# Kernel optimization log

Hardware: AMD Instinct MI355X
Metric: run time of the kernel (lower is better)

Reference implementation:

```python
import jax, jax.numpy as jnp
import numpy as np

B, T, V, E_DIM, M_DIM, H = 32, 256, 10000, 300, 128, 256


def setup_inputs() -> dict:
    key = jax.random.key(0)
    ks = jax.random.split(key, 8)
    sc = 0.05
    words = jax.random.randint(ks[0], (B, T), 0, V)            # int token ids, 0 = pad
    midis = jax.random.normal(ks[1], (B, T, M_DIM), dtype=jnp.float32)
    E  = jax.random.normal(ks[2], (V, E_DIM), dtype=jnp.float32) * sc   # embedding table
    Wm = jax.random.normal(ks[3], (M_DIM, E_DIM), dtype=jnp.float32) * sc  # midi Dense
    bm = jnp.zeros((E_DIM,), jnp.float32)
    Wx = jax.random.normal(ks[4], (E_DIM, 3 * H), dtype=jnp.float32) * sc  # GRU input kernel [z|r|h]
    bx = jnp.zeros((3 * H,), jnp.float32)
    U  = jax.random.normal(ks[5], (H, 3 * H), dtype=jnp.float32) * sc      # GRU recurrent kernel
    bu = jnp.zeros((3 * H,), jnp.float32)                                  # recurrent bias (reset_after)
    Wo = jax.random.normal(ks[6], (H, V), dtype=jnp.float32) * sc          # output Dense
    bo = jnp.zeros((V,), jnp.float32)
    return {"words": words, "midis": midis, "E": E, "Wm": Wm, "bm": bm,
            "Wx": Wx, "bx": bx, "U": U, "bu": bu, "Wo": Wo, "bo": bo}


def _gru_masked(x, mask, Wx, bx, U, bu):
    """Keras GRU (reset_after=True) with mask carry-through. x: [B,T,E], mask: [B,T] bool."""
    gx = x @ Wx + bx                      # [B,T,3H] precomputed input gates
    gx_t = jnp.swapaxes(gx, 0, 1)         # [T,B,3H]
    m_t = mask.T                          # [T,B]
    h0 = jnp.zeros((x.shape[0], H), x.dtype)

    def step(h, inp):
        g, m = inp
        gh = h @ U + bu                   # [B,3H]
        xz, xr, xn = jnp.split(g, 3, axis=-1)
        hz, hr, hn = jnp.split(gh, 3, axis=-1)
        z = jax.nn.sigmoid(xz + hz)
        r = jax.nn.sigmoid(xr + hr)
        n = jnp.tanh(xn + r * hn)         # reset_after: r applied to recurrent projection
        h_new = z * h + (1.0 - z) * n
        h_new = jnp.where(m[:, None], h_new, h)  # masked step: carry state/output
        return h_new, h_new

    h_last, seq = jax.lax.scan(step, h0, (gx_t, m_t))
    return jnp.swapaxes(seq, 0, 1), h_last  # [B,T,H], [B,H]


def reference(words, midis, E, Wm, bm, Wx, bx, U, bu, Wo, bo):
    mask = words != 0                      # Embedding(mask_zero=True).compute_mask
    x = E[words] + (midis @ Wm + bm)       # [B,T,E] fused embedding + dense add
    seq, _ = _gru_masked(x, mask, Wx, bx, U, bu)
    return seq @ Wo + bo                   # [B,T,V] logits
```

## Files before the change

### kernel.cpp

```cpp
#include <hip/hip_runtime.h>
#include <hip/hip_fp16.h>

typedef unsigned short ushort_t;
typedef short bf16x8 __attribute__((ext_vector_type(8)));
typedef float f32x4 __attribute__((ext_vector_type(4)));

#define B_SZ 32
#define T_SZ 256
#define V_SZ 10000
#define E_DIM 300
#define M_DIM 128
#define H_SZ 256

__device__ __forceinline__ ushort_t f2bf(float f) {
  unsigned u = __float_as_uint(f);
  unsigned r = u + 0x7fffu + ((u >> 16) & 1u);
  return (ushort_t)(r >> 16);
}

__global__ void k_cast_bf16(const float* __restrict__ in, ushort_t* __restrict__ out, int n) {
  int i = blockIdx.x * blockDim.x + threadIdx.x;
  if (i < n) out[i] = f2bf(in[i]);
}

template <int MODE>
__global__ void k_transpose_cast(const float* __restrict__ in, ushort_t* __restrict__ out,
                                 int R, int C, int Rp, int Cp) {
  __shared__ float tile[32][33];
  int c0 = blockIdx.x * 32, r0 = blockIdx.y * 32;
  int tx = threadIdx.x, ty = threadIdx.y;
#pragma unroll
  for (int i = 0; i < 32; i += 8) {
    int r = r0 + ty + i, c = c0 + tx;
    tile[ty + i][tx] = (r < R && c < C) ? in[(size_t)r * C + c] : 0.f;
  }
  __syncthreads();
#pragma unroll
  for (int i = 0; i < 32; i += 8) {
    int c = c0 + ty + i, r = r0 + tx;
    if (c < Cp && r < Rp) {
      float v = tile[tx][ty + i];
      if (MODE == 0) {
        out[(size_t)c * Rp + r] = f2bf(v);
      } else {
        __half h = __float2half(v);
        out[(size_t)c * Rp + r] = *(ushort_t*)&h;
      }
    }
  }
}

__global__ void k_xfuse(const float* __restrict__ xtmp, const float* __restrict__ E,
                        const int* __restrict__ words, ushort_t* __restrict__ xb) {
  int m = blockIdx.x;
  int kp = threadIdx.x;
  int w = words[m];
  float v = 0.f;
  if (kp < E_DIM) v = xtmp[(size_t)m * 320 + kp] + E[(size_t)w * E_DIM + kp];
  xb[(size_t)m * 320 + kp] = f2bf(v);
}

__global__ __launch_bounds__(256, 2) void k_gemm_bt(
    const ushort_t* __restrict__ A, const ushort_t* __restrict__ BT,
    const float* __restrict__ bias, float* __restrict__ C,
    int M, int K, int Nreal, int ldc) {
  __shared__ __align__(16) char smem[32768];
  char* As = smem;
  char* Bs = smem + 16384;
  const int tid = threadIdx.x;
  const int lane = tid & 63;
  const int w = tid >> 6;
  const int wr = w >> 1, wc = w & 1;
  const int m0 = blockIdx.x * 128;
  const int n0 = blockIdx.y * 128;

  f32x4 acc[4][4];
#pragma unroll
  for (int i = 0; i < 4; ++i)
#pragma unroll
    for (int j = 0; j < 4; ++j) acc[i][j] = (f32x4){0.f, 0.f, 0.f, 0.f};

  const int srow = tid >> 3;
  const int sc16 = tid & 7;

  for (int k0 = 0; k0 < K; k0 += 64) {
    __syncthreads();
#pragma unroll
    for (int it = 0; it < 4; ++it) {
      int row = srow + it * 32;
      int slot = sc16 ^ (row & 7);
      bf16x8 va = *(const bf16x8*)(A + (size_t)(m0 + row) * K + k0 + sc16 * 8);
      *(bf16x8*)(As + row * 128 + (slot << 4)) = va;
      bf16x8 vb = *(const bf16x8*)(BT + (size_t)(n0 + row) * K + k0 + sc16 * 8);
      *(bf16x8*)(Bs + row * 128 + (slot << 4)) = vb;
    }
    __syncthreads();

    bf16x8 af[4][2], bfr[4][2];
#pragma unroll
    for (int mi = 0; mi < 4; ++mi) {
      int r = wr * 64 + mi * 16 + (lane & 15);
#pragma unroll
      for (int kk = 0; kk < 2; ++kk) {
        int c16 = kk * 4 + (lane >> 4);
        af[mi][kk] = *(const bf16x8*)(As + r * 128 + ((c16 ^ (r & 7)) << 4));
      }
    }
#pragma unroll
    for (int ni = 0; ni < 4; ++ni) {
      int r = wc * 64 + ni * 16 + (lane & 15);
#pragma unroll
      for (int kk = 0; kk < 2; ++kk) {
        int c16 = kk * 4 + (lane >> 4);
        bfr[ni][kk] = *(const bf16x8*)(Bs + r * 128 + ((c16 ^ (r & 7)) << 4));
      }
    }
#pragma unroll
    for (int mi = 0; mi < 4; ++mi)
#pragma unroll
      for (int ni = 0; ni < 4; ++ni)
#pragma unroll
        for (int kk = 0; kk < 2; ++kk)
          acc[mi][ni] = __builtin_amdgcn_mfma_f32_16x16x32_bf16(af[mi][kk], bfr[ni][kk],
                                                                acc[mi][ni], 0, 0, 0);
  }

  const int rbase = m0 + wr * 64 + (lane >> 4) * 4;
  const int cbase = n0 + wc * 64 + (lane & 15);
#pragma unroll
  for (int ni = 0; ni < 4; ++ni) {
    int n = cbase + ni * 16;
    if (n < Nreal) {
      float bn = bias[n];
#pragma unroll
      for (int mi = 0; mi < 4; ++mi) {
#pragma unroll
        for (int rg = 0; rg < 4; ++rg) {
          int mrow = rbase + mi * 16 + rg;
          C[(size_t)mrow * ldc + n] = acc[mi][ni][rg] + bn;
        }
      }
    }
  }
}

__global__ __launch_bounds__(768, 3) void k_gru(
    const float* __restrict__ gx, const ushort_t* __restrict__ UT,
    const float* __restrict__ bu, const int* __restrict__ words,
    ushort_t* __restrict__ seqb) {
  const int b = blockIdx.x;
  const int j = threadIdx.x;
  __shared__ __align__(16) __half hbuf[H_SZ];
  __shared__ float rbuf[H_SZ];
  __shared__ float hnbuf[H_SZ];

  const __half2* Uc = (const __half2*)(UT + (size_t)j * H_SZ);
  __half2 Ur[128];
#pragma unroll
  for (int k = 0; k < 128; ++k) Ur[k] = Uc[k];
  const float bu_j = bu[j];

  float h_old = 0.f;
  if (j < H_SZ) hbuf[j] = __float2half(0.f);
  __syncthreads();

  const float4* hb4 = (const float4*)hbuf;
  for (int t = 0; t < T_SZ; ++t) {
    const size_t row = (size_t)b * T_SZ + t;
    const float* gxr = gx + row * 768;
    const int wv = words[row];
    float gxv = gxr[j];
    float xn = (j < H_SZ) ? gxr[2 * H_SZ + j] : 0.f;

    __half2 a0 = __float2half2_rn(0.f), a1 = a0;
#pragma unroll
    for (int k4 = 0; k4 < 32; ++k4) {
      float4 hv = hb4[k4];
      const __half2* hp = (const __half2*)(&hv);
      a0 = __hfma2(Ur[4 * k4 + 0], hp[0], a0);
      a1 = __hfma2(Ur[4 * k4 + 1], hp[1], a1);
      a0 = __hfma2(Ur[4 * k4 + 2], hp[2], a0);
      a1 = __hfma2(Ur[4 * k4 + 3], hp[3], a1);
    }
    float2 s0 = __half22float2(a0), s1 = __half22float2(a1);
    float gh = s0.x + s0.y + s1.x + s1.y + bu_j;

    float z = 0.f;
    if (j >= 2 * H_SZ) {
      hnbuf[j - 2 * H_SZ] = gh;
    } else if (j >= H_SZ) {
      rbuf[j - H_SZ] = 1.f / (1.f + __expf(-(gxv + gh)));
    } else {
      z = 1.f / (1.f + __expf(-(gxv + gh)));
    }
    __syncthreads();
    if (j < H_SZ) {
      float ni = xn + rbuf[j] * hnbuf[j];
      float n = 2.f / (1.f + __expf(-2.f * ni)) - 1.f;
      float hnew = (wv != 0) ? (z * h_old + (1.f - z) * n) : h_old;
      h_old = hnew;
      seqb[row * H_SZ + j] = f2bf(hnew);
      hbuf[j] = __float2half(hnew);
    }
    __syncthreads();
  }
}

extern "C" void kernel_launch(void* const* d_in, const int* in_sizes, int n_in,
                              void* d_out, int out_size, void* d_ws, size_t ws_size,
                              hipStream_t stream) {
  const int*   words = (const int*)d_in[0];
  const float* midis = (const float*)d_in[1];
  const float* E     = (const float*)d_in[2];
  const float* Wm    = (const float*)d_in[3];
  const float* bm    = (const float*)d_in[4];
  const float* Wx    = (const float*)d_in[5];
  const float* bx    = (const float*)d_in[6];
  const float* U     = (const float*)d_in[7];
  const float* bu    = (const float*)d_in[8];
  const float* Wo    = (const float*)d_in[9];
  const float* bo    = (const float*)d_in[10];
  float* out = (float*)d_out;

  const int MT = B_SZ * T_SZ;
  size_t off = 0;
  auto alloc = [&](size_t bytes) -> void* {
    void* p = (char*)d_ws + off;
    off += (bytes + 255) & ~(size_t)255;
    return p;
  };
  ushort_t* mid_b = (ushort_t*)alloc((size_t)MT * 128 * 2);
  ushort_t* WmT   = (ushort_t*)alloc((size_t)384 * 128 * 2);
  float*    xtmp  = (float*)   alloc((size_t)MT * 320 * 4);
  ushort_t* x_b   = (ushort_t*)alloc((size_t)MT * 320 * 2);
  ushort_t* WxT   = (ushort_t*)alloc((size_t)768 * 320 * 2);
  float*    gx    = (float*)   alloc((size_t)MT * 768 * 4);
  ushort_t* UT    = (ushort_t*)alloc((size_t)768 * 256 * 2);
  ushort_t* seq_b = (ushort_t*)alloc((size_t)MT * 256 * 2);
  ushort_t* WoT   = (ushort_t*)alloc((size_t)10112 * 256 * 2);
  (void)ws_size;

  k_cast_bf16<<<(MT * 128 + 255) / 256, 256, 0, stream>>>(midis, mid_b, MT * 128);
  k_transpose_cast<0><<<dim3(12, 4),  dim3(32, 8), 0, stream>>>(Wm, WmT, 128, 300, 128, 384);
  k_transpose_cast<0><<<dim3(24, 10), dim3(32, 8), 0, stream>>>(Wx, WxT, 300, 768, 320, 768);
  k_transpose_cast<0><<<dim3(316, 8), dim3(32, 8), 0, stream>>>(Wo, WoT, 256, 10000, 256, 10112);
  k_transpose_cast<1><<<dim3(24, 8),  dim3(32, 8), 0, stream>>>(U, UT, 256, 768, 256, 768);

  k_gemm_bt<<<dim3(64, 3), 256, 0, stream>>>(mid_b, WmT, bm, xtmp, MT, 128, 300, 320);
  k_xfuse<<<MT, 320, 0, stream>>>(xtmp, E, words, x_b);
  k_gemm_bt<<<dim3(64, 6), 256, 0, stream>>>(x_b, WxT, bx, gx, MT, 320, 768, 768);
  k_gru<<<B_SZ, 768, 0, stream>>>(gx, UT, bu, words, seq_b);
  k_gemm_bt<<<dim3(64, 79), 256, 0, stream>>>(seq_b, WoT, bo, out, MT, 256, 10000, 10000);
}
```

Measured before the change: 506.7 us.

## Prefetch GRU gate inputs, double-buffer hidden state, use fdot2 with fp32 accumulation

In the recurrent GRU kernel, the next timestep's precomputed input gates are loaded one step ahead, so global-memory latency overlaps with the current matvec. Word ids are staged into shared memory once per block. The hidden-state buffer is double-buffered. The packed-half FMAs are replaced by v_dot2 fp32-accumulating dot products across four independent accumulators, which improves accuracy and instruction-level parallelism but adds register pressure from the prefetched values.

New measurement: 502.9 us. About the same (-0.8%).

```diff
diff --git a/kernel.cpp b/kernel.cpp
--- a/kernel.cpp
+++ b/kernel.cpp
@@ -4,6 +4,7 @@
 typedef unsigned short ushort_t;
 typedef short bf16x8 __attribute__((ext_vector_type(8)));
 typedef float f32x4 __attribute__((ext_vector_type(4)));
+typedef _Float16 h2v __attribute__((ext_vector_type(2)));
 
 #define B_SZ 32
 #define T_SZ 256
@@ -150,40 +151,47 @@
     ushort_t* __restrict__ seqb) {
   const int b = blockIdx.x;
   const int j = threadIdx.x;
-  __shared__ __align__(16) __half hbuf[H_SZ];
+  __shared__ __align__(16) _Float16 hbuf[2][H_SZ];
   __shared__ float rbuf[H_SZ];
   __shared__ float hnbuf[H_SZ];
-
-  const __half2* Uc = (const __half2*)(UT + (size_t)j * H_SZ);
-  __half2 Ur[128];
+  __shared__ int words_s[T_SZ];
+
+  const h2v* Uc = (const h2v*)(UT + (size_t)j * H_SZ);
+  h2v Ur[128];
 #pragma unroll
   for (int k = 0; k < 128; ++k) Ur[k] = Uc[k];
   const float bu_j = bu[j];
 
+  if (j < H_SZ) hbuf[0][j] = (_Float16)0.f;
+  if (j < T_SZ) words_s[j] = words[b * T_SZ + j];
+  __syncthreads();
+
+  const float* gxp = gx + (size_t)b * T_SZ * 768;
+  float gxv = gxp[j];
+  float xn = (j < H_SZ) ? gxp[2 * H_SZ + j] : 0.f;
   float h_old = 0.f;
-  if (j < H_SZ) hbuf[j] = __float2half(0.f);
-  __syncthreads();
-
-  const float4* hb4 = (const float4*)hbuf;
+  int p = 0;
+
   for (int t = 0; t < T_SZ; ++t) {
-    const size_t row = (size_t)b * T_SZ + t;
-    const float* gxr = gx + row * 768;
-    const int wv = words[row];
-    float gxv = gxr[j];
-    float xn = (j < H_SZ) ? gxr[2 * H_SZ + j] : 0.f;
-
-    __half2 a0 = __float2half2_rn(0.f), a1 = a0;
+    float gxv_n = 0.f, xn_n = 0.f;
+    if (t + 1 < T_SZ) {
+      const float* gxr1 = gxp + (size_t)(t + 1) * 768;
+      gxv_n = gxr1[j];
+      if (j < H_SZ) xn_n = gxr1[2 * H_SZ + j];
+    }
+
+    const float4* hb4 = (const float4*)hbuf[p];
+    float a0 = 0.f, a1 = 0.f, a2 = 0.f, a3 = 0.f;
 #pragma unroll
     for (int k4 = 0; k4 < 32; ++k4) {
       float4 hv = hb4[k4];
-      const __half2* hp = (const __half2*)(&hv);
-      a0 = __hfma2(Ur[4 * k4 + 0], hp[0], a0);
-      a1 = __hfma2(Ur[4 * k4 + 1], hp[1], a1);
-      a0 = __hfma2(Ur[4 * k4 + 2], hp[2], a0);
-      a1 = __hfma2(Ur[4 * k4 + 3], hp[3], a1);
-    }
-    float2 s0 = __half22float2(a0), s1 = __half22float2(a1);
-    float gh = s0.x + s0.y + s1.x + s1.y + bu_j;
+      const h2v* hp = (const h2v*)(&hv);
+      a0 = __builtin_amdgcn_fdot2(Ur[4 * k4 + 0], hp[0], a0, false);
+      a1 = __builtin_amdgcn_fdot2(Ur[4 * k4 + 1], hp[1], a1, false);
+      a2 = __builtin_amdgcn_fdot2(Ur[4 * k4 + 2], hp[2], a2, false);
+      a3 = __builtin_amdgcn_fdot2(Ur[4 * k4 + 3], hp[3], a3, false);
+    }
+    float gh = (a0 + a1) + (a2 + a3) + bu_j;
 
     float z = 0.f;
     if (j >= 2 * H_SZ) {
@@ -197,12 +205,15 @@
     if (j < H_SZ) {
       float ni = xn + rbuf[j] * hnbuf[j];
       float n = 2.f / (1.f + __expf(-2.f * ni)) - 1.f;
-      float hnew = (wv != 0) ? (z * h_old + (1.f - z) * n) : h_old;
+      float hnew = (words_s[t] != 0) ? (z * h_old + (1.f - z) * n) : h_old;
       h_old = hnew;
-      seqb[row * H_SZ + j] = f2bf(hnew);
-      hbuf[j] = __float2half(hnew);
-    }
-    __syncthreads();
+      seqb[((size_t)b * T_SZ + t) * H_SZ + j] = f2bf(hnew);
+      hbuf[p ^ 1][j] = (_Float16)hnew;
+    }
+    __syncthreads();
+    gxv = gxv_n;
+    xn = xn_n;
+    p ^= 1;
   }
 }
 
```

## Compute GRU recurrent matvec with fp16 MFMA and register-resident U fragments

Applied to the files above, without the earlier changes.

The per-step h@U product in the GRU kernel moves from per-thread half2 FMA dot products over 768 threads to MFMA 16x16x32 f16 instructions across 8 waves. The hidden state sits as row 0 of a padded 16-row LDS tile, and U fragments stay in registers. Gate math is merged into the first 256 threads, words are staged in LDS, and next-step gx values are prefetched to hide global latency. The MFMA wastes 15 of 16 rows, and its fp32 accumulation changes numerics slightly compared with the old fp16 accumulation.

New measurement: 464.6 us. 8.3% less time.

```diff
diff --git a/kernel.cpp b/kernel.cpp
--- a/kernel.cpp
+++ b/kernel.cpp
@@ -4,6 +4,7 @@
 typedef unsigned short ushort_t;
 typedef short bf16x8 __attribute__((ext_vector_type(8)));
 typedef float f32x4 __attribute__((ext_vector_type(4)));
+typedef _Float16 f16x8 __attribute__((ext_vector_type(8)));
 
 #define B_SZ 32
 #define T_SZ 256
@@ -144,65 +145,98 @@
   }
 }
 
-__global__ __launch_bounds__(768, 3) void k_gru(
+__global__ __launch_bounds__(512, 2) void k_gru(
     const float* __restrict__ gx, const ushort_t* __restrict__ UT,
     const float* __restrict__ bu, const int* __restrict__ words,
     ushort_t* __restrict__ seqb) {
   const int b = blockIdx.x;
-  const int j = threadIdx.x;
-  __shared__ __align__(16) __half hbuf[H_SZ];
-  __shared__ float rbuf[H_SZ];
-  __shared__ float hnbuf[H_SZ];
-
-  const __half2* Uc = (const __half2*)(UT + (size_t)j * H_SZ);
-  __half2 Ur[128];
-#pragma unroll
-  for (int k = 0; k < 128; ++k) Ur[k] = Uc[k];
-  const float bu_j = bu[j];
-
+  const int tid = threadIdx.x;
+  const int lane = tid & 63;
+  const int w = tid >> 6;
+
+  __shared__ __align__(16) _Float16 hlds[16 * 256];
+  __shared__ float ghbuf[768];
+  __shared__ int words_s[T_SZ];
+
+  for (int i = tid; i < 16 * 256; i += 512) hlds[i] = (_Float16)0.f;
+  if (tid < T_SZ) words_s[tid] = words[b * T_SZ + tid];
+
+  f16x8 Ufrag[6][8];
+  {
+    const int n0 = w * 96;
+    const ushort_t* src = UT + (size_t)(n0 + (lane & 15)) * 256 + (lane >> 4) * 8;
+#pragma unroll
+    for (int ni = 0; ni < 6; ++ni) {
+#pragma unroll
+      for (int kk = 0; kk < 8; ++kk)
+        Ufrag[ni][kk] = *(const f16x8*)(src + (size_t)ni * 16 * 256 + kk * 32);
+    }
+  }
+  float buz = 0.f, bur = 0.f, bun = 0.f;
+  if (tid < H_SZ) {
+    buz = bu[tid];
+    bur = bu[H_SZ + tid];
+    bun = bu[2 * H_SZ + tid];
+  }
+  __syncthreads();
+
+  const float* gxp = gx + (size_t)b * T_SZ * 768;
+  float gxz = 0.f, gxr = 0.f, gxn = 0.f;
+  if (tid < H_SZ) {
+    gxz = gxp[tid];
+    gxr = gxp[H_SZ + tid];
+    gxn = gxp[2 * H_SZ + tid];
+  }
   float h_old = 0.f;
-  if (j < H_SZ) hbuf[j] = __float2half(0.f);
-  __syncthreads();
-
-  const float4* hb4 = (const float4*)hbuf;
+
+  const int arow = lane & 15;
+  const int abase = arow * 512;
+  const int asub = lane >> 4;
+  const int aswz = arow & 7;
+
   for (int t = 0; t < T_SZ; ++t) {
-    const size_t row = (size_t)b * T_SZ + t;
-    const float* gxr = gx + row * 768;
-    const int wv = words[row];
-    float gxv = gxr[j];
-    float xn = (j < H_SZ) ? gxr[2 * H_SZ + j] : 0.f;
-
-    __half2 a0 = __float2half2_rn(0.f), a1 = a0;
-#pragma unroll
-    for (int k4 = 0; k4 < 32; ++k4) {
-      float4 hv = hb4[k4];
-      const __half2* hp = (const __half2*)(&hv);
-      a0 = __hfma2(Ur[4 * k4 + 0], hp[0], a0);
-      a1 = __hfma2(Ur[4 * k4 + 1], hp[1], a1);
-      a0 = __hfma2(Ur[4 * k4 + 2], hp[2], a0);
-      a1 = __hfma2(Ur[4 * k4 + 3], hp[3], a1);
-    }
-    float2 s0 = __half22float2(a0), s1 = __half22float2(a1);
-    float gh = s0.x + s0.y + s1.x + s1.y + bu_j;
-
-    float z = 0.f;
-    if (j >= 2 * H_SZ) {
-      hnbuf[j - 2 * H_SZ] = gh;
-    } else if (j >= H_SZ) {
-      rbuf[j - H_SZ] = 1.f / (1.f + __expf(-(gxv + gh)));
-    } else {
-      z = 1.f / (1.f + __expf(-(gxv + gh)));
-    }
-    __syncthreads();
-    if (j < H_SZ) {
-      float ni = xn + rbuf[j] * hnbuf[j];
-      float n = 2.f / (1.f + __expf(-2.f * ni)) - 1.f;
-      float hnew = (wv != 0) ? (z * h_old + (1.f - z) * n) : h_old;
+    float gxz_n = 0.f, gxr_n = 0.f, gxn_n = 0.f;
+    if (t + 1 < T_SZ && tid < H_SZ) {
+      const float* g1 = gxp + (size_t)(t + 1) * 768;
+      gxz_n = g1[tid];
+      gxr_n = g1[H_SZ + tid];
+      gxn_n = g1[2 * H_SZ + tid];
+    }
+
+    f32x4 acc[6];
+#pragma unroll
+    for (int ni = 0; ni < 6; ++ni) acc[ni] = (f32x4){0.f, 0.f, 0.f, 0.f};
+#pragma unroll
+    for (int kk = 0; kk < 8; ++kk) {
+      int c = kk * 4 + asub;
+      f16x8 afrag = *(const f16x8*)((const char*)hlds + abase + ((c ^ aswz) << 4));
+#pragma unroll
+      for (int ni = 0; ni < 6; ++ni)
+        acc[ni] = __builtin_amdgcn_mfma_f32_16x16x32_f16(afrag, Ufrag[ni][kk], acc[ni], 0, 0, 0);
+    }
+    if (lane < 16) {
+      const int nb = w * 96 + lane;
+#pragma unroll
+      for (int ni = 0; ni < 6; ++ni) ghbuf[nb + ni * 16] = acc[ni][0];
+    }
+    __syncthreads();
+
+    if (tid < H_SZ) {
+      float hz = ghbuf[tid] + buz;
+      float hr = ghbuf[H_SZ + tid] + bur;
+      float hn = ghbuf[2 * H_SZ + tid] + bun;
+      float z = 1.f / (1.f + __expf(-(gxz + hz)));
+      float r = 1.f / (1.f + __expf(-(gxr + hr)));
+      float nv = 2.f / (1.f + __expf(-2.f * (gxn + r * hn))) - 1.f;
+      float hnew = (words_s[t] != 0) ? (z * h_old + (1.f - z) * nv) : h_old;
       h_old = hnew;
-      seqb[row * H_SZ + j] = f2bf(hnew);
-      hbuf[j] = __float2half(hnew);
-    }
-    __syncthreads();
+      seqb[((size_t)b * T_SZ + t) * H_SZ + tid] = f2bf(hnew);
+      hlds[tid] = (_Float16)hnew;
+    }
+    __syncthreads();
+    gxz = gxz_n;
+    gxr = gxr_n;
+    gxn = gxn_n;
   }
 }
 
@@ -249,6 +283,6 @@
   k_gemm_bt<<<dim3(64, 3), 256, 0, stream>>>(mid_b, WmT, bm, xtmp, MT, 128, 300, 320);
   k_xfuse<<<MT, 320, 0, stream>>>(xtmp, E, words, x_b);
   k_gemm_bt<<<dim3(64, 6), 256, 0, stream>>>(x_b, WxT, bx, gx, MT, 320, 768, 768);
-  k_gru<<<B_SZ, 768, 0, stream>>>(gx, UT, bu, words, seq_b);
+  k_gru<<<B_SZ, 512, 0, stream>>>(gx, UT, bu, words, seq_b);
   k_gemm_bt<<<dim3(64, 79), 256, 0, stream>>>(seq_b, WoT, bo, out, MT, 256, 10000, 10000);
 }
```
